# Kernel optimization log

Hardware: AMD Instinct MI355X
Metric: run time of the kernel (lower is better)

Reference implementation:

```python
import jax, jax.numpy as jnp
import numpy as np

B, C, H, W = 8, 384, 32, 32
NUM_HEADS = 8
HEAD_DIM = C // NUM_HEADS


def setup_inputs() -> dict:
    key = jax.random.key(0)
    k1, k2, k3, k4, k5 = jax.random.split(key, 5)
    s = 1.0 / np.sqrt(C)
    return {
        "x": jax.random.normal(k1, (B, C, H, W), dtype=jnp.float32),
        "w_qkv": jax.random.normal(k2, (3 * C, C), dtype=jnp.float32) * s,   # 1x1 conv == linear over channels
        "b_qkv": jax.random.normal(k3, (3 * C,), dtype=jnp.float32) * 0.01,
        "w_proj": jax.random.normal(k4, (C, C), dtype=jnp.float32) * s,
        "b_proj": jax.random.normal(k5, (C,), dtype=jnp.float32) * 0.01,
    }


def reference(x, w_qkv, b_qkv, w_proj, b_proj):
    b, c, h, w = x.shape
    n = h * w
    scale = HEAD_DIM ** (-0.5)
    # 1x1 conv qkv: (B, 3C, H, W)
    qkv = jnp.einsum('bchw,oc->bohw', x, w_qkv) + b_qkv[None, :, None, None]
    # 'b (three hd d) h0 w0 -> three b hd (h0 w0) d'
    qkv = qkv.reshape(b, 3, NUM_HEADS, HEAD_DIM, n)
    qkv = jnp.transpose(qkv, (1, 0, 2, 4, 3))  # (3, B, heads, N, d)
    q, k, v = qkv[0], qkv[1], qkv[2]
    attn = jnp.einsum('bhnd,bhmd->bhnm', q, k) * scale
    attn = jax.nn.softmax(attn, axis=-1)
    out = jnp.einsum('bhnm,bhmd->bhnd', attn, v)          # (B, heads, N, d)
    out = jnp.transpose(out, (0, 1, 3, 2)).reshape(b, c, h, w)  # b (hd d) h w
    out = jnp.einsum('bchw,oc->bohw', out, w_proj) + b_proj[None, :, None, None]
    return out
```

## Files before the change

### kernel.cpp

```cpp
#include <hip/hip_runtime.h>
#include <hip/hip_bf16.h>

typedef __hip_bfloat16 bf16;
typedef __bf16 bfx8 __attribute__((ext_vector_type(8)));
typedef float f32x4 __attribute__((ext_vector_type(4)));

#define Bk   8
#define Ck   384
#define NHk  8
#define Dk   48
#define Dp   64
#define Nk   1024
#define O3   1152


__global__ __launch_bounds__(256) void xpose_kernel(
    const float* __restrict__ x, bf16* __restrict__ Xs)
{
    __shared__ bf16 tile[32][33];
    const int b = blockIdx.z, c0 = blockIdx.y * 32, n0 = blockIdx.x * 32;
    const int tn = threadIdx.x & 31, tc = threadIdx.x >> 5;
    const float* xb = x + (size_t)b * Ck * Nk;
    #pragma unroll
    for (int i = 0; i < 4; ++i)
        tile[tc + 8 * i][tn] = __float2bfloat16(xb[(size_t)(c0 + tc + 8 * i) * Nk + n0 + tn]);
    __syncthreads();
    bf16* base = Xs + ((size_t)b * 64 + (n0 >> 4)) * 48 * 128 + (c0 >> 3) * 128;
    #pragma unroll
    for (int i = 0; i < 4; ++i) {
        int n_loc = tc + 8 * i, c_loc = tn;
        base[(size_t)(n_loc >> 4) * 6144 + (c_loc >> 3) * 128 +
             (n_loc & 15) * 8 + (c_loc & 7)] = tile[c_loc][n_loc];
    }
}

__global__ __launch_bounds__(256) void wconv_kernel(
    const float* __restrict__ wq, const float* __restrict__ wp,
    bf16* __restrict__ Wq, bf16* __restrict__ Wp,
    bf16* __restrict__ Qs, bf16* __restrict__ Ks)
{
    int i = blockIdx.x * 256 + threadIdx.x;
    if (i < O3 * Ck) {
        int o = i / Ck, c = i - o * Ck;
        Wq[((size_t)(o >> 4) * 48 + (c >> 3)) * 128 + (o & 15) * 8 + (c & 7)] =
            __float2bfloat16(wq[i]);
    }
    if (i < Ck * Ck) {
        int o = i / Ck, c = i - o * Ck;
        Wp[((size_t)(o >> 4) * 48 + (c >> 3)) * 128 + (o & 15) * 8 + (c & 7)] =
            __float2bfloat16(wp[i]);
    }
    if (i < 262144) {
        int buf = i >> 17;
        int r17 = i & 131071;
        int head = r17 >> 11;
        int r11 = r17 & 2047;
        int g = r11 >> 5, c5 = r11 & 31;
        int cd = 6 + (c5 >> 4), e = c5 & 15;
        bf16* p = (buf ? Ks : Qs) + (size_t)head * 65536 +
                  ((size_t)g * 8 + cd) * 128 + e * 8;
        *(int4*)p = (int4){0, 0, 0, 0};
    }
}

__global__ __launch_bounds__(256) void qkv_mfma_kernel(
    const bf16* __restrict__ Xs, const bf16* __restrict__ Wq,
    const float* __restrict__ bias,
    bf16* __restrict__ Qs, bf16* __restrict__ Ks, bf16* __restrict__ Vs)
{
    const int b    = blockIdx.z;
    const int by   = blockIdx.y;
    const int bx   = blockIdx.x;
    const int o0   = by * 64;
    const int n0   = bx * 128;
    const int wave = threadIdx.x >> 6;
    const int lane = threadIdx.x & 63;
    const int l15  = lane & 15, quad = lane >> 4;
    const int t3   = o0 / Ck;

    const bf16* xg[2];
    const bf16* wg[4];
    #pragma unroll
    for (int i = 0; i < 2; ++i)
        xg[i] = Xs + ((size_t)(b * 64 + bx * 8 + wave * 2 + i) * 48) * 128 + lane * 8;
    #pragma unroll
    for (int j = 0; j < 4; ++j)
        wg[j] = Wq + ((size_t)(by * 4 + j) * 48) * 128 + lane * 8;

    f32x4 acc[8];
    #pragma unroll
    for (int i = 0; i < 8; ++i) acc[i] = (f32x4){0.f, 0.f, 0.f, 0.f};

    if (t3 < 2) {
        #pragma unroll
        for (int s = 0; s < 12; ++s) {
            bfx8 fx[2], fw[4];
            #pragma unroll
            for (int i = 0; i < 2; ++i) fx[i] = *(const bfx8*)(xg[i] + s * 512);
            #pragma unroll
            for (int j = 0; j < 4; ++j) fw[j] = *(const bfx8*)(wg[j] + s * 512);
            #pragma unroll
            for (int i = 0; i < 2; ++i)
                #pragma unroll
                for (int j = 0; j < 4; ++j)
                    acc[i * 4 + j] = __builtin_amdgcn_mfma_f32_16x16x32_bf16(
                        fx[i], fw[j], acc[i * 4 + j], 0, 0, 0);
        }
        const float qscale = 0.2082350964f;
        #pragma unroll
        for (int j = 0; j < 4; ++j) {
            int o  = o0 + j * 16 + l15;
            float bi = bias[o];
            int r  = o - t3 * Ck;
            int hd = r / Dk, d = r - hd * Dk;
            bf16* hb = (t3 == 0 ? Qs : Ks) + (size_t)(b * NHk + hd) * 65536
                     + (d >> 3) * 128 + (d & 7);
            #pragma unroll
            for (int i = 0; i < 2; ++i) {
                #pragma unroll
                for (int reg = 0; reg < 4; ++reg) {
                    int npos = n0 + wave * 32 + i * 16 + quad * 4 + reg;
                    float v = acc[i * 4 + j][reg] + bi;
                    if (t3 == 0) v *= qscale;
                    hb[(size_t)(npos >> 4) * 1024 + (npos & 15) * 8] = __float2bfloat16(v);
                }
            }
        }
    } else {
        #pragma unroll
        for (int s = 0; s < 12; ++s) {
            bfx8 fx[2], fw[4];
            #pragma unroll
            for (int i = 0; i < 2; ++i) fx[i] = *(const bfx8*)(xg[i] + s * 512);
            #pragma unroll
            for (int j = 0; j < 4; ++j) fw[j] = *(const bfx8*)(wg[j] + s * 512);
            #pragma unroll
            for (int j = 0; j < 4; ++j)
                #pragma unroll
                for (int i = 0; i < 2; ++i)
                    acc[j * 2 + i] = __builtin_amdgcn_mfma_f32_16x16x32_bf16(
                        fw[j], fx[i], acc[j * 2 + i], 0, 0, 0);
        }
        #pragma unroll
        for (int j = 0; j < 4; ++j) {
            #pragma unroll
            for (int reg = 0; reg < 4; ++reg) {
                int o  = o0 + j * 16 + quad * 4 + reg;
                float bi = bias[o];
                int r  = o - 2 * Ck;
                int hd = r / Dk, d = r - hd * Dk;
                bf16* vb = Vs + (size_t)(b * NHk + hd) * 49152
                         + ((size_t)(d >> 4) * 128) * 128 + (d & 15) * 8;
                #pragma unroll
                for (int i = 0; i < 2; ++i) {
                    int npos = n0 + wave * 32 + i * 16 + l15;
                    vb[(size_t)(npos >> 3) * 128 + (npos & 7)] =
                        __float2bfloat16(acc[j * 2 + i][reg] + bi);
                }
            }
        }
    }
}

__global__ __launch_bounds__(256) void attn_kernel(
    const bf16* __restrict__ Qs, const bf16* __restrict__ Ks,
    const bf16* __restrict__ Vs, bf16* __restrict__ AO)
{
    __shared__ __align__(16) short Ps[4 * 16 * 72];
    __shared__ float sums[4][16];

    const int bx   = blockIdx.x;
    const int hd   = blockIdx.y;
    const int b    = blockIdx.z;
    const int t    = threadIdx.x;
    const int wave = t >> 6;
    const int lane = t & 63;
    const int l15  = lane & 15;
    const int quad = lane >> 4;
    const int grp  = bx * 4 + wave;

    const bf16* qb = Qs + (size_t)(b * NHk + hd) * 65536;
    const bf16* kb = Ks + (size_t)(b * NHk + hd) * 65536;
    const bf16* vb = Vs + (size_t)(b * NHk + hd) * 49152;

    const bf16* qp = qb + ((size_t)grp * 8 + quad) * 128 + l15 * 8;
    const bfx8 bq0 = *(const bfx8*)(qp);
    const bfx8 bq1 = *(const bfx8*)(qp + 512);

    float l_run = 0.f;
    f32x4 oacc[3];
    #pragma unroll
    for (int dc = 0; dc < 3; ++dc) oacc[dc] = (f32x4){0.f, 0.f, 0.f, 0.f};

    short* PsW = Ps + wave * 16 * 72;

    for (int k0 = 0; k0 < Nk; k0 += 64) {
        f32x4 sf[4];
        #pragma unroll
        for (int s = 0; s < 4; ++s) {
            const bf16* kp = kb + ((size_t)((k0 >> 4) + s) * 8 + quad) * 128 + l15 * 8;
            const bfx8 kf0 = *(const bfx8*)(kp);
            const bfx8 kf1 = *(const bfx8*)(kp + 512);
            f32x4 z = (f32x4){0.f, 0.f, 0.f, 0.f};
            z = __builtin_amdgcn_mfma_f32_16x16x32_bf16(kf0, bq0, z, 0, 0, 0);
            z = __builtin_amdgcn_mfma_f32_16x16x32_bf16(kf1, bq1, z, 0, 0, 0);
            sf[s] = z;
        }

        float lsum = 0.f;
        #pragma unroll
        for (int s = 0; s < 4; ++s) {
            ushort4 pk;
            float e0 = __builtin_amdgcn_exp2f(sf[s][0]);
            float e1 = __builtin_amdgcn_exp2f(sf[s][1]);
            float e2 = __builtin_amdgcn_exp2f(sf[s][2]);
            float e3 = __builtin_amdgcn_exp2f(sf[s][3]);
            lsum += (e0 + e1) + (e2 + e3);
            bf16 h0 = __float2bfloat16(e0), h1 = __float2bfloat16(e1);
            bf16 h2 = __float2bfloat16(e2), h3 = __float2bfloat16(e3);
            pk.x = *(unsigned short*)&h0; pk.y = *(unsigned short*)&h1;
            pk.z = *(unsigned short*)&h2; pk.w = *(unsigned short*)&h3;
            *(ushort4*)&PsW[l15 * 72 + s * 16 + quad * 4] = pk;
        }
        l_run += lsum;

        asm volatile("s_waitcnt lgkmcnt(0)" ::: "memory");

        const bfx8 ap0 = *(const bfx8*)&PsW[l15 * 72 + quad * 8];
        const bfx8 ap1 = *(const bfx8*)&PsW[l15 * 72 + 32 + quad * 8];
        #pragma unroll
        for (int dc = 0; dc < 3; ++dc) {
            const bf16* vp = vb + ((size_t)dc * 128 + (k0 >> 3) + quad) * 128 + l15 * 8;
            const bfx8 bv0 = *(const bfx8*)(vp);
            const bfx8 bv1 = *(const bfx8*)(vp + 512);
            oacc[dc] = __builtin_amdgcn_mfma_f32_16x16x32_bf16(ap0, bv0, oacc[dc], 0, 0, 0);
            oacc[dc] = __builtin_amdgcn_mfma_f32_16x16x32_bf16(ap1, bv1, oacc[dc], 0, 0, 0);
        }
    }

    {
        float lt = l_run;
        lt += __shfl_xor(lt, 16, 64);
        lt += __shfl_xor(lt, 32, 64);
        sums[wave][l15] = lt;
    }
    asm volatile("s_waitcnt lgkmcnt(0)" ::: "memory");

    short* OsW = PsW;
    #pragma unroll
    for (int r = 0; r < 4; ++r) {
        int qi = quad * 4 + r;
        float rli = 1.0f / sums[wave][qi];
        #pragma unroll
        for (int dcc = 0; dcc < 3; ++dcc) {
            bf16 hb = __float2bfloat16(oacc[dcc][r] * rli);
            OsW[qi * 64 + dcc * 16 + l15] = *(short*)&hb;
        }
    }
    asm volatile("s_waitcnt lgkmcnt(0)" ::: "memory");

    bf16* aob = AO + (((size_t)b * 64 + grp) * 48 + hd * 6) * 128;
    {
        int u = lane;
        int4 v = *(const int4*)&OsW[(u & 15) * 64 + (u >> 4) * 8];
        *(int4*)(aob + u * 8) = v;
        if (lane < 32) {
            int u2 = 64 + lane;
            int4 v2 = *(const int4*)&OsW[(u2 & 15) * 64 + (u2 >> 4) * 8];
            *(int4*)(aob + u2 * 8) = v2;
        }
    }
}

__global__ __launch_bounds__(256) void proj_mfma_kernel(
    const bf16* __restrict__ AO, const bf16* __restrict__ Wp,
    const float* __restrict__ bias, float* __restrict__ out)
{
    const int b    = blockIdx.z;
    const int by   = blockIdx.y;
    const int bx   = blockIdx.x;
    const int o0   = by * 64;
    const int n0   = bx * 128;
    const int wave = threadIdx.x >> 6;
    const int lane = threadIdx.x & 63;
    const int l15  = lane & 15, quad = lane >> 4;

    const bf16* ag[2];
    const bf16* wg[4];
    #pragma unroll
    for (int i = 0; i < 2; ++i)
        ag[i] = AO + ((size_t)(b * 64 + bx * 8 + wave * 2 + i) * 48) * 128 + lane * 8;
    #pragma unroll
    for (int j = 0; j < 4; ++j)
        wg[j] = Wp + ((size_t)(by * 4 + j) * 48) * 128 + lane * 8;

    f32x4 acc[8];
    #pragma unroll
    for (int i = 0; i < 8; ++i) acc[i] = (f32x4){0.f, 0.f, 0.f, 0.f};

    #pragma unroll
    for (int s = 0; s < 12; ++s) {
        bfx8 fx[2], fw[4];
        #pragma unroll
        for (int i = 0; i < 2; ++i) fx[i] = *(const bfx8*)(ag[i] + s * 512);
        #pragma unroll
        for (int j = 0; j < 4; ++j) fw[j] = *(const bfx8*)(wg[j] + s * 512);
        #pragma unroll
        for (int j = 0; j < 4; ++j)
            #pragma unroll
            for (int i = 0; i < 2; ++i)
                acc[j * 2 + i] = __builtin_amdgcn_mfma_f32_16x16x32_bf16(
                    fw[j], fx[i], acc[j * 2 + i], 0, 0, 0);
    }

    #pragma unroll
    for (int j = 0; j < 4; ++j) {
        #pragma unroll
        for (int reg = 0; reg < 4; ++reg) {
            int o  = o0 + j * 16 + quad * 4 + reg;
            float bi = bias[o];
            #pragma unroll
            for (int i = 0; i < 2; ++i) {
                int npos = n0 + wave * 32 + i * 16 + l15;
                out[((size_t)b * Ck + o) * Nk + npos] = acc[j * 2 + i][reg] + bi;
            }
        }
    }
}

extern "C" void kernel_launch(void* const* d_in, const int* in_sizes, int n_in,
                              void* d_out, int out_size, void* d_ws, size_t ws_size,
                              hipStream_t stream)
{
    const float* x      = (const float*)d_in[0];
    const float* w_qkv  = (const float*)d_in[1];
    const float* b_qkv  = (const float*)d_in[2];
    const float* w_proj = (const float*)d_in[3];
    const float* b_proj = (const float*)d_in[4];
    float* out = (float*)d_out;

    const size_t XT_SEG = (size_t)Bk * Nk * Ck;
    const size_t WQ_SEG = (size_t)O3 * Ck;
    const size_t WP_SEG = (size_t)Ck * Ck;
    const size_t QK_SEG = (size_t)Bk * NHk * Nk * Dp;
    const size_t V_SEG  = (size_t)Bk * NHk * Dk * Nk;

    bf16* Xs = (bf16*)d_ws;
    bf16* Wq = Xs + XT_SEG;
    bf16* Wp = Wq + WQ_SEG;
    bf16* Qs = Wp + WP_SEG;
    bf16* Ks = Qs + QK_SEG;
    bf16* Vs = Ks + QK_SEG;
    bf16* AO = Vs + V_SEG;

    xpose_kernel<<<dim3(Nk / 32, Ck / 32, Bk), 256, 0, stream>>>(x, Xs);
    wconv_kernel<<<(O3 * Ck + 255) / 256, 256, 0, stream>>>(
        w_qkv, w_proj, Wq, Wp, Qs, Ks);
    qkv_mfma_kernel<<<dim3(Nk / 128, O3 / 64, Bk), 256, 0, stream>>>(
        Xs, Wq, b_qkv, Qs, Ks, Vs);
    attn_kernel<<<dim3(16, NHk, Bk), 256, 0, stream>>>(Qs, Ks, Vs, AO);
    proj_mfma_kernel<<<dim3(Nk / 128, Ck / 64, Bk), 256, 0, stream>>>(
        AO, Wp, b_proj, out);
}
```

Before: 136.0 us.

## Process two query tiles per wave with K register double-buffering in attention

Each attention wave now handles two 16-row query tiles, so every K and V fragment loaded from global memory feeds twice the MFMA work. K fragments for the next 64-key chunk are prefetched into a second register set while the current chunk is computed, and V loads are issued at the top of each step. The grid is reordered so heads and batch vary fastest, block count is halved, and launch bounds request two blocks per CU. The cost is higher register pressure and fewer blocks, which may reduce occupancy or cause spills.

```diff
diff --git a/kernel.cpp b/kernel.cpp
--- a/kernel.cpp
+++ b/kernel.cpp
@@ -162,105 +162,147 @@
     }
 }
 
-__global__ __launch_bounds__(256) void attn_kernel(
+__global__ __launch_bounds__(256, 2) void attn_kernel(
     const bf16* __restrict__ Qs, const bf16* __restrict__ Ks,
     const bf16* __restrict__ Vs, bf16* __restrict__ AO)
 {
-    __shared__ __align__(16) short Ps[4 * 16 * 72];
-    __shared__ float sums[4][16];
-
-    const int bx   = blockIdx.x;
-    const int hd   = blockIdx.y;
-    const int b    = blockIdx.z;
+    __shared__ __align__(16) short Ps[4 * 2 * 16 * 72];
+    __shared__ float sums[4][2][16];
+
+    const int hd   = blockIdx.x;
+    const int b    = blockIdx.y;
+    const int bx   = blockIdx.z;
     const int t    = threadIdx.x;
     const int wave = t >> 6;
     const int lane = t & 63;
     const int l15  = lane & 15;
     const int quad = lane >> 4;
-    const int grp  = bx * 4 + wave;
+    const int grp16 = (bx * 4 + wave) * 2;
 
     const bf16* qb = Qs + (size_t)(b * NHk + hd) * 65536;
     const bf16* kb = Ks + (size_t)(b * NHk + hd) * 65536;
     const bf16* vb = Vs + (size_t)(b * NHk + hd) * 49152;
 
-    const bf16* qp = qb + ((size_t)grp * 8 + quad) * 128 + l15 * 8;
-    const bfx8 bq0 = *(const bfx8*)(qp);
-    const bfx8 bq1 = *(const bfx8*)(qp + 512);
-
-    float l_run = 0.f;
-    f32x4 oacc[3];
-    #pragma unroll
-    for (int dc = 0; dc < 3; ++dc) oacc[dc] = (f32x4){0.f, 0.f, 0.f, 0.f};
-
-    short* PsW = Ps + wave * 16 * 72;
-
-    for (int k0 = 0; k0 < Nk; k0 += 64) {
-        f32x4 sf[4];
+    bfx8 bq[2][2];
+    #pragma unroll
+    for (int qt = 0; qt < 2; ++qt) {
+        const bf16* qp = qb + ((size_t)(grp16 + qt) * 8 + quad) * 128 + l15 * 8;
+        bq[qt][0] = *(const bfx8*)(qp);
+        bq[qt][1] = *(const bfx8*)(qp + 512);
+    }
+
+    float l_run[2] = {0.f, 0.f};
+    f32x4 oacc[2][3];
+    #pragma unroll
+    for (int qt = 0; qt < 2; ++qt)
+        #pragma unroll
+        for (int dc = 0; dc < 3; ++dc) oacc[qt][dc] = (f32x4){0.f, 0.f, 0.f, 0.f};
+
+    short* const PsW[2] = { Ps + wave * 2304, Ps + wave * 2304 + 1152 };
+
+    auto loadK = [&](bfx8* kf, int k0) {
+        const bf16* kp0 = kb + (size_t)k0 * 64 + quad * 128 + l15 * 8;
         #pragma unroll
         for (int s = 0; s < 4; ++s) {
-            const bf16* kp = kb + ((size_t)((k0 >> 4) + s) * 8 + quad) * 128 + l15 * 8;
-            const bfx8 kf0 = *(const bfx8*)(kp);
-            const bfx8 kf1 = *(const bfx8*)(kp + 512);
-            f32x4 z = (f32x4){0.f, 0.f, 0.f, 0.f};
-            z = __builtin_amdgcn_mfma_f32_16x16x32_bf16(kf0, bq0, z, 0, 0, 0);
-            z = __builtin_amdgcn_mfma_f32_16x16x32_bf16(kf1, bq1, z, 0, 0, 0);
-            sf[s] = z;
-        }
-
-        float lsum = 0.f;
+            kf[2 * s]     = *(const bfx8*)(kp0 + s * 1024);
+            kf[2 * s + 1] = *(const bfx8*)(kp0 + s * 1024 + 512);
+        }
+    };
+    auto loadV = [&](bfx8* vf, int k0) {
+        const bf16* vp0 = vb + ((size_t)(k0 >> 3) + quad) * 128 + l15 * 8;
+        #pragma unroll
+        for (int dc = 0; dc < 3; ++dc) {
+            vf[2 * dc]     = *(const bfx8*)(vp0 + (size_t)dc * 16384);
+            vf[2 * dc + 1] = *(const bfx8*)(vp0 + (size_t)dc * 16384 + 512);
+        }
+    };
+
+    auto step = [&](const bfx8* kf, bfx8* kfn, int k0, bool pf) {
+        bfx8 vf[6];
+        loadV(vf, k0);
+        if (pf) loadK(kfn, k0 + 64);
+
+        f32x4 sf[2][4];
         #pragma unroll
         for (int s = 0; s < 4; ++s) {
-            ushort4 pk;
-            float e0 = __builtin_amdgcn_exp2f(sf[s][0]);
-            float e1 = __builtin_amdgcn_exp2f(sf[s][1]);
-            float e2 = __builtin_amdgcn_exp2f(sf[s][2]);
-            float e3 = __builtin_amdgcn_exp2f(sf[s][3]);
-            lsum += (e0 + e1) + (e2 + e3);
-            bf16 h0 = __float2bfloat16(e0), h1 = __float2bfloat16(e1);
-            bf16 h2 = __float2bfloat16(e2), h3 = __float2bfloat16(e3);
-            pk.x = *(unsigned short*)&h0; pk.y = *(unsigned short*)&h1;
-            pk.z = *(unsigned short*)&h2; pk.w = *(unsigned short*)&h3;
-            *(ushort4*)&PsW[l15 * 72 + s * 16 + quad * 4] = pk;
-        }
-        l_run += lsum;
-
-        asm volatile("s_waitcnt lgkmcnt(0)" ::: "memory");
-
-        const bfx8 ap0 = *(const bfx8*)&PsW[l15 * 72 + quad * 8];
-        const bfx8 ap1 = *(const bfx8*)&PsW[l15 * 72 + 32 + quad * 8];
-        #pragma unroll
-        for (int dc = 0; dc < 3; ++dc) {
-            const bf16* vp = vb + ((size_t)dc * 128 + (k0 >> 3) + quad) * 128 + l15 * 8;
-            const bfx8 bv0 = *(const bfx8*)(vp);
-            const bfx8 bv1 = *(const bfx8*)(vp + 512);
-            oacc[dc] = __builtin_amdgcn_mfma_f32_16x16x32_bf16(ap0, bv0, oacc[dc], 0, 0, 0);
-            oacc[dc] = __builtin_amdgcn_mfma_f32_16x16x32_bf16(ap1, bv1, oacc[dc], 0, 0, 0);
-        }
-    }
-
-    {
-        float lt = l_run;
+            #pragma unroll
+            for (int qt = 0; qt < 2; ++qt) {
+                f32x4 z = (f32x4){0.f, 0.f, 0.f, 0.f};
+                z = __builtin_amdgcn_mfma_f32_16x16x32_bf16(kf[2 * s],     bq[qt][0], z, 0, 0, 0);
+                z = __builtin_amdgcn_mfma_f32_16x16x32_bf16(kf[2 * s + 1], bq[qt][1], z, 0, 0, 0);
+                sf[qt][s] = z;
+            }
+        }
+
+        #pragma unroll
+        for (int qt = 0; qt < 2; ++qt) {
+            float lsum = 0.f;
+            #pragma unroll
+            for (int s = 0; s < 4; ++s) {
+                ushort4 pk;
+                float e0 = __builtin_amdgcn_exp2f(sf[qt][s][0]);
+                float e1 = __builtin_amdgcn_exp2f(sf[qt][s][1]);
+                float e2 = __builtin_amdgcn_exp2f(sf[qt][s][2]);
+                float e3 = __builtin_amdgcn_exp2f(sf[qt][s][3]);
+                lsum += (e0 + e1) + (e2 + e3);
+                bf16 h0 = __float2bfloat16(e0), h1 = __float2bfloat16(e1);
+                bf16 h2 = __float2bfloat16(e2), h3 = __float2bfloat16(e3);
+                pk.x = *(unsigned short*)&h0; pk.y = *(unsigned short*)&h1;
+                pk.z = *(unsigned short*)&h2; pk.w = *(unsigned short*)&h3;
+                *(ushort4*)&PsW[qt][l15 * 72 + s * 16 + quad * 4] = pk;
+            }
+            l_run[qt] += lsum;
+        }
+
+        #pragma unroll
+        for (int qt = 0; qt < 2; ++qt) {
+            const bfx8 ap0 = *(const bfx8*)&PsW[qt][l15 * 72 + quad * 8];
+            const bfx8 ap1 = *(const bfx8*)&PsW[qt][l15 * 72 + 32 + quad * 8];
+            #pragma unroll
+            for (int dc = 0; dc < 3; ++dc) {
+                oacc[qt][dc] = __builtin_amdgcn_mfma_f32_16x16x32_bf16(
+                    ap0, vf[2 * dc], oacc[qt][dc], 0, 0, 0);
+                oacc[qt][dc] = __builtin_amdgcn_mfma_f32_16x16x32_bf16(
+                    ap1, vf[2 * dc + 1], oacc[qt][dc], 0, 0, 0);
+            }
+        }
+    };
+
+    bfx8 kfA[8], kfB[8];
+    loadK(kfA, 0);
+    #pragma unroll 1
+    for (int k0 = 0; k0 < Nk; k0 += 128) {
+        step(kfA, kfB, k0, true);
+        step(kfB, kfA, k0 + 64, k0 + 128 < Nk);
+    }
+
+    #pragma unroll
+    for (int qt = 0; qt < 2; ++qt) {
+        float lt = l_run[qt];
         lt += __shfl_xor(lt, 16, 64);
         lt += __shfl_xor(lt, 32, 64);
-        sums[wave][l15] = lt;
-    }
-    asm volatile("s_waitcnt lgkmcnt(0)" ::: "memory");
-
-    short* OsW = PsW;
-    #pragma unroll
-    for (int r = 0; r < 4; ++r) {
-        int qi = quad * 4 + r;
-        float rli = 1.0f / sums[wave][qi];
-        #pragma unroll
-        for (int dcc = 0; dcc < 3; ++dcc) {
-            bf16 hb = __float2bfloat16(oacc[dcc][r] * rli);
-            OsW[qi * 64 + dcc * 16 + l15] = *(short*)&hb;
-        }
-    }
-    asm volatile("s_waitcnt lgkmcnt(0)" ::: "memory");
-
-    bf16* aob = AO + (((size_t)b * 64 + grp) * 48 + hd * 6) * 128;
-    {
+        sums[wave][qt][l15] = lt;
+    }
+
+    #pragma unroll
+    for (int qt = 0; qt < 2; ++qt) {
+        short* OsW = PsW[qt];
+        #pragma unroll
+        for (int r = 0; r < 4; ++r) {
+            int qi = quad * 4 + r;
+            float rli = 1.0f / sums[wave][qt][qi];
+            #pragma unroll
+            for (int dcc = 0; dcc < 3; ++dcc) {
+                bf16 hb = __float2bfloat16(oacc[qt][dcc][r] * rli);
+                OsW[qi * 64 + dcc * 16 + l15] = *(short*)&hb;
+            }
+        }
+    }
+
+    #pragma unroll
+    for (int qt = 0; qt < 2; ++qt) {
+        bf16* aob = AO + (((size_t)b * 64 + grp16 + qt) * 48 + hd * 6) * 128;
+        short* OsW = PsW[qt];
         int u = lane;
         int4 v = *(const int4*)&OsW[(u & 15) * 64 + (u >> 4) * 8];
         *(int4*)(aob + u * 8) = v;
@@ -358,7 +400,7 @@
         w_qkv, w_proj, Wq, Wp, Qs, Ks);
     qkv_mfma_kernel<<<dim3(Nk / 128, O3 / 64, Bk), 256, 0, stream>>>(
         Xs, Wq, b_qkv, Qs, Ks, Vs);
-    attn_kernel<<<dim3(16, NHk, Bk), 256, 0, stream>>>(Qs, Ks, Vs, AO);
+    attn_kernel<<<dim3(NHk, Bk, 8), 256, 0, stream>>>(Qs, Ks, Vs, AO);
     proj_mfma_kernel<<<dim3(Nk / 128, Ck / 64, Bk), 256, 0, stream>>>(
         AO, Wp, b_proj, out);
 }
```

After: 125.8 us. 1.08x faster.
